# Kernel optimization log

Hardware: AMD Instinct MI355X
Metric: run time of the kernel (lower is better)

## Reference

```python
import jax, jax.numpy as jnp
import numpy as np

POOL_SIZE = 7
NUM_ROIS = 300


def setup_inputs() -> dict:
    key = jax.random.key(0)
    k1, k2, k3 = jax.random.split(key, 3)
    img = jax.random.normal(k1, (1, 256, 256, 512), dtype=jnp.float32)
    # rois: [x, y, w, h] integer-valued (the layer casts them to int32 anyway)
    xy = jax.random.randint(k2, (1, NUM_ROIS, 2), 0, 192)   # x, y in [0, 192)
    wh = jax.random.randint(k3, (1, NUM_ROIS, 2), 8, 64)    # w, h in [8, 64) -> x+w <= 255
    rois = jnp.concatenate([xy, wh], axis=-1).astype(jnp.int32)
    return {"img": img, "rois": rois}


def _axis_coords(start, size, pool_size):
    """Half-pixel-center bilinear source coords for one axis of a crop.
    Returns absolute gather indices (lo, hi) into the full feature map and lerp frac."""
    scale = size.astype(jnp.float32) / pool_size
    src = (jnp.arange(pool_size, dtype=jnp.float32) + 0.5) * scale - 0.5
    src = jnp.clip(src, 0.0, size.astype(jnp.float32) - 1.0)
    i0 = jnp.floor(src).astype(jnp.int32)
    i1 = jnp.minimum(i0 + 1, size - 1)
    frac = src - i0.astype(jnp.float32)
    return start + i0, start + i1, frac


def _roi_resize(feat, roi, pool_size):
    # feat: (H, W, C); roi: (4,) int32 [x, y, w, h]
    x, y, w, h = roi[0], roi[1], roi[2], roi[3]
    y0, y1, fy = _axis_coords(y, h, pool_size)  # (P,)
    x0, x1, fx = _axis_coords(x, w, pool_size)  # (P,)
    r0 = feat[y0]  # (P, W, C)
    r1 = feat[y1]  # (P, W, C)
    wx = fx[None, :, None]
    rows0 = r0[:, x0] * (1.0 - wx) + r0[:, x1] * wx  # (P, P, C)
    rows1 = r1[:, x0] * (1.0 - wx) + r1[:, x1] * wx
    wy = fy[:, None, None]
    return rows0 * (1.0 - wy) + rows1 * wy  # (P, P, C)


def reference(img, rois):
    # channels_last path: per-ROI crop + bilinear resize to (P, P)
    pooled = jax.vmap(lambda r: _roi_resize(img[0], r, POOL_SIZE))(rois[0])
    return pooled[None]  # (1, num_rois, P, P, C)
```

## Files before the change

### kernel.cpp

```cpp
#include <hip/hip_runtime.h>

#define POOL 7
#define NUM_ROIS 300
#define CHANNELS 512
#define IMG_W 256

__global__ __launch_bounds__(128) void roi_align_kernel(
    const float* __restrict__ img,
    const int* __restrict__ rois,
    float* __restrict__ out)
{
    const int bid = blockIdx.x;
    const int r   = bid / (POOL * POOL);
    const int pp  = bid % (POOL * POOL);
    const int py  = pp / POOL;
    const int px  = pp % POOL;

    const int x = rois[r * 4 + 0];
    const int y = rois[r * 4 + 1];
    const int w = rois[r * 4 + 2];
    const int h = rois[r * 4 + 3];

    float scy  = (float)h / (float)POOL;
    float srcy = ((float)py + 0.5f) * scy - 0.5f;
    srcy = fminf(fmaxf(srcy, 0.0f), (float)h - 1.0f);
    int   iy0 = (int)floorf(srcy);
    int   iy1 = min(iy0 + 1, h - 1);
    float fy  = srcy - (float)iy0;
    const int y0 = y + iy0, y1 = y + iy1;

    float scx  = (float)w / (float)POOL;
    float srcx = ((float)px + 0.5f) * scx - 0.5f;
    srcx = fminf(fmaxf(srcx, 0.0f), (float)w - 1.0f);
    int   ix0 = (int)floorf(srcx);
    int   ix1 = min(ix0 + 1, w - 1);
    float fx  = srcx - (float)ix0;
    const int x0 = x + ix0, x1 = x + ix1;

    const float4* p00 = (const float4*)(img + ((size_t)y0 * IMG_W + x0) * CHANNELS);
    const float4* p01 = (const float4*)(img + ((size_t)y0 * IMG_W + x1) * CHANNELS);
    const float4* p10 = (const float4*)(img + ((size_t)y1 * IMG_W + x0) * CHANNELS);
    const float4* p11 = (const float4*)(img + ((size_t)y1 * IMG_W + x1) * CHANNELS);
    float4* po = (float4*)(out + (((size_t)r * POOL + py) * POOL + px) * CHANNELS);

    const int t = threadIdx.x;

    float4 a = p00[t];
    float4 b = p01[t];
    float4 c = p10[t];
    float4 d = p11[t];

    const float gx = 1.0f - fx;
    const float gy = 1.0f - fy;

    float4 o;
    o.x = (a.x * gx + b.x * fx) * gy + (c.x * gx + d.x * fx) * fy;
    o.y = (a.y * gx + b.y * fx) * gy + (c.y * gx + d.y * fx) * fy;
    o.z = (a.z * gx + b.z * fx) * gy + (c.z * gx + d.z * fx) * fy;
    o.w = (a.w * gx + b.w * fx) * gy + (c.w * gx + d.w * fx) * fy;

    po[t] = o;
}

extern "C" void kernel_launch(void* const* d_in, const int* in_sizes, int n_in,
                              void* d_out, int out_size, void* d_ws, size_t ws_size,
                              hipStream_t stream) {
    const float* img  = (const float*)d_in[0];
    const int*   rois = (const int*)d_in[1];
    float*       out  = (float*)d_out;

    const int nblocks = NUM_ROIS * POOL * POOL;
    roi_align_kernel<<<nblocks, 128, 0, stream>>>(img, rois, out);
}
```

Before: 27.14 us.

## Process a full output row per block with batched loads and nontemporal stores

Each block now computes one pooled row (7 output pixels) of an ROI instead of a single pixel, so the grid shrinks by a factor of 7. The ROI coordinate math is shared across the row, and all 28 float4 gathers are issued before any arithmetic to raise memory-level parallelism per thread. Outputs are written with nontemporal stores to avoid polluting the cache. In exchange, register pressure is higher and there are fewer blocks to spread across the GPU's compute units.

Result: no change. 27.06 us (-0.3%).

```diff
diff --git a/kernel.cpp b/kernel.cpp
--- a/kernel.cpp
+++ b/kernel.cpp
@@ -5,16 +5,16 @@
 #define CHANNELS 512
 #define IMG_W 256
 
-__global__ __launch_bounds__(128) void roi_align_kernel(
+typedef float f32x4 __attribute__((ext_vector_type(4)));
+
+__global__ __launch_bounds__(128) void roi_align_row_kernel(
     const float* __restrict__ img,
     const int* __restrict__ rois,
     float* __restrict__ out)
 {
     const int bid = blockIdx.x;
-    const int r   = bid / (POOL * POOL);
-    const int pp  = bid % (POOL * POOL);
-    const int py  = pp / POOL;
-    const int px  = pp % POOL;
+    const int r   = bid / POOL;
+    const int py  = bid % POOL;
 
     const int x = rois[r * 4 + 0];
     const int y = rois[r * 4 + 1];
@@ -26,40 +26,43 @@
     srcy = fminf(fmaxf(srcy, 0.0f), (float)h - 1.0f);
     int   iy0 = (int)floorf(srcy);
     int   iy1 = min(iy0 + 1, h - 1);
-    float fy  = srcy - (float)iy0;
-    const int y0 = y + iy0, y1 = y + iy1;
+    const float fy = srcy - (float)iy0;
+    const float gy = 1.0f - fy;
+    const size_t row0 = (size_t)(y + iy0) * IMG_W;
+    const size_t row1 = (size_t)(y + iy1) * IMG_W;
 
-    float scx  = (float)w / (float)POOL;
-    float srcx = ((float)px + 0.5f) * scx - 0.5f;
-    srcx = fminf(fmaxf(srcx, 0.0f), (float)w - 1.0f);
-    int   ix0 = (int)floorf(srcx);
-    int   ix1 = min(ix0 + 1, w - 1);
-    float fx  = srcx - (float)ix0;
-    const int x0 = x + ix0, x1 = x + ix1;
-
-    const float4* p00 = (const float4*)(img + ((size_t)y0 * IMG_W + x0) * CHANNELS);
-    const float4* p01 = (const float4*)(img + ((size_t)y0 * IMG_W + x1) * CHANNELS);
-    const float4* p10 = (const float4*)(img + ((size_t)y1 * IMG_W + x0) * CHANNELS);
-    const float4* p11 = (const float4*)(img + ((size_t)y1 * IMG_W + x1) * CHANNELS);
-    float4* po = (float4*)(out + (((size_t)r * POOL + py) * POOL + px) * CHANNELS);
+    const float scx = (float)w / (float)POOL;
+    int   x0[POOL], x1[POOL];
+    float fx[POOL];
+#pragma unroll
+    for (int px = 0; px < POOL; ++px) {
+        float srcx = ((float)px + 0.5f) * scx - 0.5f;
+        srcx = fminf(fmaxf(srcx, 0.0f), (float)w - 1.0f);
+        int i0 = (int)floorf(srcx);
+        int i1 = min(i0 + 1, w - 1);
+        fx[px] = srcx - (float)i0;
+        x0[px] = x + i0;
+        x1[px] = x + i1;
+    }
 
     const int t = threadIdx.x;
 
-    float4 a = p00[t];
-    float4 b = p01[t];
-    float4 c = p10[t];
-    float4 d = p11[t];
+    f32x4 a[POOL], b[POOL], c[POOL], d[POOL];
+#pragma unroll
+    for (int px = 0; px < POOL; ++px) {
+        a[px] = ((const f32x4*)(img + (row0 + (size_t)x0[px]) * CHANNELS))[t];
+        b[px] = ((const f32x4*)(img + (row0 + (size_t)x1[px]) * CHANNELS))[t];
+        c[px] = ((const f32x4*)(img + (row1 + (size_t)x0[px]) * CHANNELS))[t];
+        d[px] = ((const f32x4*)(img + (row1 + (size_t)x1[px]) * CHANNELS))[t];
+    }
 
-    const float gx = 1.0f - fx;
-    const float gy = 1.0f - fy;
-
-    float4 o;
-    o.x = (a.x * gx + b.x * fx) * gy + (c.x * gx + d.x * fx) * fy;
-    o.y = (a.y * gx + b.y * fx) * gy + (c.y * gx + d.y * fx) * fy;
-    o.z = (a.z * gx + b.z * fx) * gy + (c.z * gx + d.z * fx) * fy;
-    o.w = (a.w * gx + b.w * fx) * gy + (c.w * gx + d.w * fx) * fy;
-
-    po[t] = o;
+    f32x4* po = (f32x4*)(out + ((size_t)r * POOL + py) * POOL * CHANNELS);
+#pragma unroll
+    for (int px = 0; px < POOL; ++px) {
+        const float f = fx[px], g = 1.0f - f;
+        f32x4 o = (a[px] * g + b[px] * f) * gy + (c[px] * g + d[px] * f) * fy;
+        __builtin_nontemporal_store(o, &po[px * (CHANNELS / 4) + t]);
+    }
 }
 
 extern "C" void kernel_launch(void* const* d_in, const int* in_sizes, int n_in,
@@ -69,6 +72,6 @@
     const int*   rois = (const int*)d_in[1];
     float*       out  = (float*)d_out;
 
-    const int nblocks = NUM_ROIS * POOL * POOL;
-    roi_align_kernel<<<nblocks, 128, 0, stream>>>(img, rois, out);
+    const int nblocks = NUM_ROIS * POOL;
+    roi_align_row_kernel<<<nblocks, 128, 0, stream>>>(img, rois, out);
 }
```
